# Kernel tuning notes

Hardware: AMD Instinct MI355X
Metric: run time of the kernel (lower is better)

Reference implementation:

```python
import jax, jax.numpy as jnp
import numpy as np


def grid_sample3d(vol, grid):
    """PyTorch-equivalent 3D grid_sample, mode='bilinear' (trilinear),
    padding_mode='zeros', align_corners=True.
    vol:  [N, C, D, H, W] float
    grid: [N, Do, Ho, Wo, 3] float in [-1, 1], coords ordered (x, y, z)
    returns [N, C, Do, Ho, Wo]
    """
    N, C, D, H, W = vol.shape
    x = grid[..., 0]
    y = grid[..., 1]
    z = grid[..., 2]
    # align_corners=True: map [-1,1] -> [0, size-1]
    ix = (x + 1.0) * 0.5 * (W - 1)
    iy = (y + 1.0) * 0.5 * (H - 1)
    iz = (z + 1.0) * 0.5 * (D - 1)

    ix0 = jnp.floor(ix)
    iy0 = jnp.floor(iy)
    iz0 = jnp.floor(iz)
    wx1 = ix - ix0  # fractional parts
    wy1 = iy - iy0
    wz1 = iz - iz0
    wx0 = 1.0 - wx1
    wy0 = 1.0 - wy1
    wz0 = 1.0 - wz1

    ix0i = ix0.astype(jnp.int32)
    iy0i = iy0.astype(jnp.int32)
    iz0i = iz0.astype(jnp.int32)
    ix1i = ix0i + 1
    iy1i = iy0i + 1
    iz1i = iz0i + 1

    v = jnp.transpose(vol, (0, 2, 3, 4, 1))  # [N, D, H, W, C] for channel-last gather
    b = jnp.arange(N)[:, None, None, None]   # batch index broadcast over [Do,Ho,Wo]

    def gather(zi, yi, xi):
        # zero padding: out-of-bounds corners contribute 0
        inb = (zi >= 0) & (zi < D) & (yi >= 0) & (yi < H) & (xi >= 0) & (xi < W)
        zc = jnp.clip(zi, 0, D - 1)
        yc = jnp.clip(yi, 0, H - 1)
        xc = jnp.clip(xi, 0, W - 1)
        vals = v[b, zc, yc, xc]  # [N, Do, Ho, Wo, C]
        return vals * inb[..., None].astype(vals.dtype)

    out = (
        gather(iz0i, iy0i, ix0i) * (wz0 * wy0 * wx0)[..., None]
        + gather(iz0i, iy0i, ix1i) * (wz0 * wy0 * wx1)[..., None]
        + gather(iz0i, iy1i, ix0i) * (wz0 * wy1 * wx0)[..., None]
        + gather(iz0i, iy1i, ix1i) * (wz0 * wy1 * wx1)[..., None]
        + gather(iz1i, iy0i, ix0i) * (wz1 * wy0 * wx0)[..., None]
        + gather(iz1i, iy0i, ix1i) * (wz1 * wy0 * wx1)[..., None]
        + gather(iz1i, iy1i, ix0i) * (wz1 * wy1 * wx0)[..., None]
        + gather(iz1i, iy1i, ix1i) * (wz1 * wy1 * wx1)[..., None]
    )  # [N, Do, Ho, Wo, C]
    return jnp.transpose(out, (0, 4, 1, 2, 3))  # [N, C, Do, Ho, Wo]


def setup_inputs() -> dict:
    key = jax.random.key(0)
    k1, k2 = jax.random.split(key)
    N, C, D, H, W = 8, 32, 64, 64, 64
    Do, Ho, Wo = 64, 64, 64
    inp = jax.random.normal(k1, (N, C, D, H, W), dtype=jnp.float32)
    grid = jax.random.uniform(k2, (N, Do, Ho, Wo, 3), dtype=jnp.float32,
                              minval=-1.0, maxval=1.0)
    return {"input": inp, "grid": grid}


def reference(input, grid):
    return grid_sample3d(input, grid)
```

## Files before the change

kernel.cpp:

```cpp
#include <hip/hip_runtime.h>

#define SVOL (64 * 64 * 64)

typedef float vfloat4 __attribute__((ext_vector_type(4)));
typedef unsigned int vuint4 __attribute__((ext_vector_type(4)));
typedef unsigned short vushort4 __attribute__((ext_vector_type(4)));

__device__ __forceinline__ unsigned short f32_to_bf16_rne(float f) {
    unsigned int u = __float_as_uint(f);
    unsigned int r = u + 0x7FFFu + ((u >> 16) & 1u);
    return (unsigned short)(r >> 16);
}

__global__ __launch_bounds__(256) void transpose_bf16_kernel(
    const float* __restrict__ vol, unsigned short* __restrict__ volT) {
    __shared__ float tile[32][257];

    const int t = threadIdx.x;
    const int n = blockIdx.y;
    const long s0 = (long)blockIdx.x * 256;

    const float* src = vol + (long)n * 32 * SVOL + s0;
    const int sl = (t & 63) * 4;
    const int cb = t >> 6;
#pragma unroll
    for (int it = 0; it < 8; ++it) {
        const int c = it * 4 + cb;
        const vfloat4 v =
            __builtin_nontemporal_load((const vfloat4*)(src + (long)c * SVOL + sl));
        tile[c][sl + 0] = v.x;
        tile[c][sl + 1] = v.y;
        tile[c][sl + 2] = v.z;
        tile[c][sl + 3] = v.w;
    }
    __syncthreads();

    unsigned short* dst = volT + ((long)n * SVOL + s0) * 32;
    const int c4 = (t & 7) * 4;
#pragma unroll
    for (int it = 0; it < 8; ++it) {
        const int sl2 = it * 32 + (t >> 3);
        vushort4 v;
        v.x = f32_to_bf16_rne(tile[c4 + 0][sl2]);
        v.y = f32_to_bf16_rne(tile[c4 + 1][sl2]);
        v.z = f32_to_bf16_rne(tile[c4 + 2][sl2]);
        v.w = f32_to_bf16_rne(tile[c4 + 3][sl2]);
        *(vushort4*)(dst + (long)sl2 * 32 + c4) = v;
    }
}

__device__ __forceinline__ void fma_bf16pair(float& a0, float& a1,
                                             unsigned int u, float w) {
    const float lo = __uint_as_float(u << 16);
    const float hi = __uint_as_float(u & 0xFFFF0000u);
    a0 = fmaf(w, lo, a0);
    a1 = fmaf(w, hi, a1);
}

__global__ __launch_bounds__(256) void gather_bf16_kernel(
    const float* __restrict__ grid, const unsigned short* __restrict__ volT,
    float* __restrict__ out) {
    const long gidx = (long)blockIdx.x * 256 + threadIdx.x;
    const int n = (int)(gidx >> 18);
    const int s = (int)(gidx & (SVOL - 1));

    const float x = __builtin_nontemporal_load(grid + gidx * 3 + 0);
    const float y = __builtin_nontemporal_load(grid + gidx * 3 + 1);
    const float z = __builtin_nontemporal_load(grid + gidx * 3 + 2);

    const float ix = (x + 1.0f) * 0.5f * 63.0f;
    const float iy = (y + 1.0f) * 0.5f * 63.0f;
    const float iz = (z + 1.0f) * 0.5f * 63.0f;

    const float fx = floorf(ix), fy = floorf(iy), fz = floorf(iz);
    const int ix0 = (int)fx, iy0 = (int)fy, iz0 = (int)fz;
    const float tx = ix - fx, ty = iy - fy, tz = iz - fz;

    float wx[2], wy[2], wz[2];
    int xc[2], yc[2], zc[2];
    wx[0] = (ix0 >= 0 && ix0 < 64) ? (1.0f - tx) : 0.0f;
    wx[1] = (ix0 + 1 >= 0 && ix0 + 1 < 64) ? tx : 0.0f;
    wy[0] = (iy0 >= 0 && iy0 < 64) ? (1.0f - ty) : 0.0f;
    wy[1] = (iy0 + 1 >= 0 && iy0 + 1 < 64) ? ty : 0.0f;
    wz[0] = (iz0 >= 0 && iz0 < 64) ? (1.0f - tz) : 0.0f;
    wz[1] = (iz0 + 1 >= 0 && iz0 + 1 < 64) ? tz : 0.0f;
    xc[0] = min(max(ix0, 0), 63);
    xc[1] = min(max(ix0 + 1, 0), 63);
    yc[0] = min(max(iy0, 0), 63);
    yc[1] = min(max(iy0 + 1, 0), 63);
    zc[0] = min(max(iz0, 0), 63);
    zc[1] = min(max(iz0 + 1, 0), 63);

    const vuint4* base = (const vuint4*)(volT + (long)n * SVOL * 32);

    float acc[32];
#pragma unroll
    for (int c = 0; c < 32; ++c) acc[c] = 0.0f;

#pragma unroll
    for (int k = 0; k < 8; ++k) {
        const int kx = k & 1;
        const int ky = (k >> 1) & 1;
        const int kz = k >> 2;
        const float w = wz[kz] * wy[ky] * wx[kx];
        const long site = (long)((zc[kz] * 64 + yc[ky]) * 64 + xc[kx]);
        const vuint4* cp = base + site * 4;
#pragma unroll
        for (int q = 0; q < 4; ++q) {
            const vuint4 v = cp[q];
            fma_bf16pair(acc[q * 8 + 0], acc[q * 8 + 1], v.x, w);
            fma_bf16pair(acc[q * 8 + 2], acc[q * 8 + 3], v.y, w);
            fma_bf16pair(acc[q * 8 + 4], acc[q * 8 + 5], v.z, w);
            fma_bf16pair(acc[q * 8 + 6], acc[q * 8 + 7], v.w, w);
        }
    }

    float* op = out + (long)n * 32 * SVOL + s;
#pragma unroll
    for (int c = 0; c < 32; ++c) {
        __builtin_nontemporal_store(acc[c], op + (long)c * SVOL);
    }
}

__global__ __launch_bounds__(256) void gather_direct_kernel(
    const float* __restrict__ grid, const float* __restrict__ vol,
    float* __restrict__ out) {
    const long gidx = (long)blockIdx.x * 256 + threadIdx.x;
    const int n = (int)(gidx >> 18);
    const int s = (int)(gidx & (SVOL - 1));

    const float* g = grid + gidx * 3;
    const float ix = (g[0] + 1.0f) * 0.5f * 63.0f;
    const float iy = (g[1] + 1.0f) * 0.5f * 63.0f;
    const float iz = (g[2] + 1.0f) * 0.5f * 63.0f;

    const float fx = floorf(ix), fy = floorf(iy), fz = floorf(iz);
    const int ix0 = (int)fx, iy0 = (int)fy, iz0 = (int)fz;
    const float tx = ix - fx, ty = iy - fy, tz = iz - fz;

    float wx[2], wy[2], wz[2];
    int xc[2], yc[2], zc[2];
    wx[0] = (ix0 >= 0 && ix0 < 64) ? (1.0f - tx) : 0.0f;
    wx[1] = (ix0 + 1 < 64) ? tx : 0.0f;
    wy[0] = (iy0 >= 0 && iy0 < 64) ? (1.0f - ty) : 0.0f;
    wy[1] = (iy0 + 1 < 64) ? ty : 0.0f;
    wz[0] = (iz0 >= 0 && iz0 < 64) ? (1.0f - tz) : 0.0f;
    wz[1] = (iz0 + 1 < 64) ? tz : 0.0f;
    xc[0] = min(max(ix0, 0), 63);
    xc[1] = min(max(ix0 + 1, 0), 63);
    yc[0] = min(max(iy0, 0), 63);
    yc[1] = min(max(iy0 + 1, 0), 63);
    zc[0] = min(max(iz0, 0), 63);
    zc[1] = min(max(iz0 + 1, 0), 63);

    long offk[8];
    float wk[8];
#pragma unroll
    for (int k = 0; k < 8; ++k) {
        const int kx = k & 1, ky = (k >> 1) & 1, kz = k >> 2;
        offk[k] = (long)(zc[kz] * 64 + yc[ky]) * 64 + xc[kx];
        wk[k] = wz[kz] * wy[ky] * wx[kx];
    }

    const float* base = vol + (long)n * 32 * SVOL;
    float* op = out + (long)n * 32 * SVOL + s;
    for (int c = 0; c < 32; ++c) {
        const float* bc = base + (long)c * SVOL;
        float a = 0.0f;
#pragma unroll
        for (int k = 0; k < 8; ++k) a = fmaf(wk[k], bc[offk[k]], a);
        op[(long)c * SVOL] = a;
    }
}

extern "C" void kernel_launch(void* const* d_in, const int* in_sizes, int n_in,
                              void* d_out, int out_size, void* d_ws, size_t ws_size,
                              hipStream_t stream) {
    const float* vol = (const float*)d_in[0];
    const float* grid = (const float*)d_in[1];
    float* out = (float*)d_out;

    const size_t needed = (size_t)8 * SVOL * 32 * sizeof(unsigned short);
    const int npoints_blocks = (8 * SVOL) / 256;

    if (ws_size >= needed) {
        unsigned short* volT = (unsigned short*)d_ws;
        transpose_bf16_kernel<<<dim3(1024, 8), 256, 0, stream>>>(vol, volT);
        gather_bf16_kernel<<<npoints_blocks, 256, 0, stream>>>(grid, volT, out);
    } else {
        gather_direct_kernel<<<npoints_blocks, 256, 0, stream>>>(grid, vol, out);
    }
}
```

Baseline: 682.5 us.

## Batch all corner gathers before accumulation and simplify transpose to per-thread registers

The gather kernel now issues all 32 vector loads for the eight corners up front, before any FMA, so memory latency overlaps across corners instead of being serialized per corner. Launch bounds are tightened to request 3 blocks per CU, which bounds register use against the larger live set of loaded values. The transpose kernel drops the LDS tile and has each thread load its 32 channel values directly with coalesced reads, pack them to bf16, and write 64 contiguous bytes. The risk is register pressure or spilling in the gather kernel and less coalesced stores in the transpose.

Measured after the change: 707.1 us. +3.6%, slower.

```diff
diff --git a/kernel.cpp b/kernel.cpp
--- a/kernel.cpp
+++ b/kernel.cpp
@@ -4,7 +4,6 @@
 
 typedef float vfloat4 __attribute__((ext_vector_type(4)));
 typedef unsigned int vuint4 __attribute__((ext_vector_type(4)));
-typedef unsigned short vushort4 __attribute__((ext_vector_type(4)));
 
 __device__ __forceinline__ unsigned short f32_to_bf16_rne(float f) {
     unsigned int u = __float_as_uint(f);
@@ -14,38 +13,34 @@
 
 __global__ __launch_bounds__(256) void transpose_bf16_kernel(
     const float* __restrict__ vol, unsigned short* __restrict__ volT) {
-    __shared__ float tile[32][257];
-
     const int t = threadIdx.x;
     const int n = blockIdx.y;
-    const long s0 = (long)blockIdx.x * 256;
-
-    const float* src = vol + (long)n * 32 * SVOL + s0;
-    const int sl = (t & 63) * 4;
-    const int cb = t >> 6;
-#pragma unroll
-    for (int it = 0; it < 8; ++it) {
-        const int c = it * 4 + cb;
-        const vfloat4 v =
-            __builtin_nontemporal_load((const vfloat4*)(src + (long)c * SVOL + sl));
-        tile[c][sl + 0] = v.x;
-        tile[c][sl + 1] = v.y;
-        tile[c][sl + 2] = v.z;
-        tile[c][sl + 3] = v.w;
-    }
-    __syncthreads();
-
-    unsigned short* dst = volT + ((long)n * SVOL + s0) * 32;
-    const int c4 = (t & 7) * 4;
-#pragma unroll
-    for (int it = 0; it < 8; ++it) {
-        const int sl2 = it * 32 + (t >> 3);
-        vushort4 v;
-        v.x = f32_to_bf16_rne(tile[c4 + 0][sl2]);
-        v.y = f32_to_bf16_rne(tile[c4 + 1][sl2]);
-        v.z = f32_to_bf16_rne(tile[c4 + 2][sl2]);
-        v.w = f32_to_bf16_rne(tile[c4 + 3][sl2]);
-        *(vushort4*)(dst + (long)sl2 * 32 + c4) = v;
+    const long s = (long)blockIdx.x * 256 + t;
+
+    const float* src = vol + (long)n * 32 * SVOL + s;
+
+    float v[32];
+#pragma unroll
+    for (int c = 0; c < 32; ++c) {
+        v[c] = __builtin_nontemporal_load(src + (long)c * SVOL);
+    }
+
+    unsigned int r[16];
+#pragma unroll
+    for (int h = 0; h < 16; ++h) {
+        r[h] = (unsigned int)f32_to_bf16_rne(v[2 * h]) |
+               ((unsigned int)f32_to_bf16_rne(v[2 * h + 1]) << 16);
+    }
+
+    vuint4* dst = (vuint4*)volT + ((long)n * SVOL + s) * 4;
+#pragma unroll
+    for (int q = 0; q < 4; ++q) {
+        vuint4 w;
+        w.x = r[4 * q + 0];
+        w.y = r[4 * q + 1];
+        w.z = r[4 * q + 2];
+        w.w = r[4 * q + 3];
+        dst[q] = w;
     }
 }
 
@@ -57,7 +52,7 @@
     a1 = fmaf(w, hi, a1);
 }
 
-__global__ __launch_bounds__(256) void gather_bf16_kernel(
+__global__ __launch_bounds__(256, 3) void gather_bf16_kernel(
     const float* __restrict__ grid, const unsigned short* __restrict__ volT,
     float* __restrict__ out) {
     const long gidx = (long)blockIdx.x * 256 + threadIdx.x;
@@ -93,21 +88,35 @@
 
     const vuint4* base = (const vuint4*)(volT + (long)n * SVOL * 32);
 
-    float acc[32];
-#pragma unroll
-    for (int c = 0; c < 32; ++c) acc[c] = 0.0f;
-
+    float wk[8];
+    const vuint4* cp[8];
 #pragma unroll
     for (int k = 0; k < 8; ++k) {
         const int kx = k & 1;
         const int ky = (k >> 1) & 1;
         const int kz = k >> 2;
-        const float w = wz[kz] * wy[ky] * wx[kx];
-        const long site = (long)((zc[kz] * 64 + yc[ky]) * 64 + xc[kx]);
-        const vuint4* cp = base + site * 4;
+        wk[k] = wz[kz] * wy[ky] * wx[kx];
+        const int site = (zc[kz] * 64 + yc[ky]) * 64 + xc[kx];
+        cp[k] = base + (long)site * 4;
+    }
+
+    vuint4 cv[8][4];
+#pragma unroll
+    for (int k = 0; k < 8; ++k) {
+#pragma unroll
+        for (int q = 0; q < 4; ++q) cv[k][q] = cp[k][q];
+    }
+
+    float acc[32];
+#pragma unroll
+    for (int c = 0; c < 32; ++c) acc[c] = 0.0f;
+
+#pragma unroll
+    for (int k = 0; k < 8; ++k) {
+        const float w = wk[k];
 #pragma unroll
         for (int q = 0; q < 4; ++q) {
-            const vuint4 v = cp[q];
+            const vuint4 v = cv[k][q];
             fma_bf16pair(acc[q * 8 + 0], acc[q * 8 + 1], v.x, w);
             fma_bf16pair(acc[q * 8 + 2], acc[q * 8 + 3], v.y, w);
             fma_bf16pair(acc[q * 8 + 4], acc[q * 8 + 5], v.z, w);
```
